# Optimization experiments

Measured on AMD Instinct MI355X. Metric: run time of the kernel, lower is better.

The kernel has to match this reference:

```python
import jax, jax.numpy as jnp
import numpy as np

H = 512  # hidden_size


def setup_inputs() -> dict:
    key = jax.random.key(0)
    ks = jax.random.split(key, 13)
    B, S, E, V = 64, 2048, 512, 32000
    s = 0.05
    return {
        "word_input": jax.random.randint(ks[0], (B,), 0, V),
        "last_hidden": jax.random.normal(ks[1], (1, B, H), jnp.float32),
        "encoder_outputs": jax.random.normal(ks[2], (S, B, H), jnp.float32),
        "emb": jax.random.normal(ks[3], (V, E), jnp.float32) * s,
        "attn_W": jax.random.normal(ks[4], (H, 2 * H), jnp.float32) * s,
        "attn_b": jax.random.normal(ks[5], (H,), jnp.float32) * s,
        "v": jax.random.normal(ks[6], (H,), jnp.float32) * s,
        "W_ih": jax.random.normal(ks[7], (3 * H, H + E), jnp.float32) * s,
        "W_hh": jax.random.normal(ks[8], (3 * H, H), jnp.float32) * s,
        "b_ih": jax.random.normal(ks[9], (3 * H,), jnp.float32) * s,
        "b_hh": jax.random.normal(ks[10], (3 * H,), jnp.float32) * s,
        "out_W": jax.random.normal(ks[11], (V, 2 * H), jnp.float32) * s,
        "out_b": jax.random.normal(ks[12], (V,), jnp.float32) * s,
    }


def reference(word_input, last_hidden, encoder_outputs, emb, attn_W, attn_b, v,
              W_ih, W_hh, b_ih, b_hh, out_W, out_b):
    # word_input: [B] int; last_hidden: [1,B,H]; encoder_outputs: [S,B,H]
    hid = last_hidden[-1]                       # [B,H]
    enc = jnp.transpose(encoder_outputs, (1, 0, 2))  # [B,S,H]

    # Bahdanau 'concat' attention: tanh(W [h;e] + b) . v  (split W to avoid [B,S,2H])
    Wa, We = attn_W[:, :H], attn_W[:, H:]
    energy = jnp.tanh((hid @ Wa.T)[:, None, :] + jnp.einsum('bsh,kh->bsk', enc, We) + attn_b)
    scores = jnp.einsum('bsk,k->bs', energy, v)       # [B,S]
    attn = jax.nn.softmax(scores, axis=1)             # [B,S]
    context = jnp.einsum('bs,bsh->bh', attn, enc)     # [B,H]

    # GRU step (PyTorch gate layout: r, z, n)
    x = jnp.concatenate([emb[word_input], context], axis=1)  # [B,E+H]
    gi = x @ W_ih.T + b_ih
    gh = hid @ W_hh.T + b_hh
    r = jax.nn.sigmoid(gi[:, :H] + gh[:, :H])
    z = jax.nn.sigmoid(gi[:, H:2 * H] + gh[:, H:2 * H])
    n = jnp.tanh(gi[:, 2 * H:] + r * gh[:, 2 * H:])
    h_new = (1.0 - z) * n + z * hid                   # [B,H]

    logits = jnp.concatenate([h_new, context], axis=1) @ out_W.T + out_b
    output = jax.nn.log_softmax(logits, axis=1)       # [B,V]
    return output, h_new[None]                        # hidden: [1,B,H]
```

## Files before the change

kernel.cpp:

```cpp
#include <hip/hip_runtime.h>
#include <hip/hip_bf16.h>
#include <cstdint>
#include <cstddef>

#define HD 512
#define BB 64
#define SS 2048
#define VV 32000
#define MM (SS*BB)
#define NCH 32

typedef __attribute__((ext_vector_type(8))) short bf16x8;
typedef __attribute__((ext_vector_type(4))) float f32x4;

static __device__ __forceinline__ unsigned pack2(float a, float b) {
    unsigned r;
    asm("v_cvt_pk_bf16_f32 %0, %1, %2" : "=v"(r) : "v"(a), "v"(b));
    return r;
}
static __device__ __forceinline__ float rcp_fast(float x) {
    float r; asm("v_rcp_f32 %0, %1" : "=v"(r) : "v"(x)); return r;
}
static __device__ __forceinline__ float tanh_fast(float x) {
    float e = __expf(2.f * x);
    return 1.f - 2.f * rcp_fast(e + 1.f);
}
static __device__ __forceinline__ float sigmoid_fast(float x) {
    return 1.f / (1.f + __expf(-x));
}
static __device__ __forceinline__ void gload16(const void* g, void* l) {
    __builtin_amdgcn_global_load_lds(
        (const __attribute__((address_space(1))) void*)g,
        (__attribute__((address_space(3))) void*)l, 16, 0, 0);
}

__global__ void prep_kernel(const float* __restrict__ hid,
                            const float* __restrict__ attn_W,
                            const float* __restrict__ attn_b,
                            float* __restrict__ qc,
                            uint4* __restrict__ WeB4) {
    int i = blockIdx.x * 256 + threadIdx.x;
    int n = i >> 6, b = i & 63;
    const float* hrow = hid + b * HD;
    const float* wrow = attn_W + (size_t)n * (2 * HD);
    float acc = 0.f;
    for (int k = 0; k < HD; k += 4) {
        float4 h4 = *(const float4*)(hrow + k);
        float4 w4 = *(const float4*)(wrow + k);
        acc += h4.x * w4.x + h4.y * w4.y + h4.z * w4.z + h4.w * w4.w;
    }
    qc[b * HD + n] = acc + attn_b[n];
    int col = (i << 3) & 511;
    int cc0 = col >> 3;
    const float* src = attn_W + (size_t)n * (2 * HD) + HD + col;
    float4 f0 = *(const float4*)(src);
    float4 f1 = *(const float4*)(src + 4);
    uint4 p;
    p.x = pack2(f0.x, f0.y); p.y = pack2(f0.z, f0.w);
    p.z = pack2(f1.x, f1.y); p.w = pack2(f1.z, f1.w);
    int ccs = (cc0 & ~7) | ((cc0 & 7) ^ (n & 7));
    WeB4[n * 64 + ccs] = p;
}

__global__ __launch_bounds__(512, 2) void fattn_kernel(
    const float* __restrict__ enc,
    const uint4* __restrict__ WeB4,
    const float* __restrict__ qc,
    const float* __restrict__ vvec,
    float* __restrict__ oP,
    float* __restrict__ lP)
{
    __shared__ char smem[8192 + 65536 + 2048 + 256];
    uint4* Ald = (uint4*)smem;
    uint4* Bld = (uint4*)(smem + 8192);
    float (*red)[8] = (float(*)[8])(smem + 8192 + 65536);
    float* p_lds = (float*)(smem + 8192 + 65536 + 2048);
    float* opart = (float*)(smem + 8192);

    const int tid = threadIdx.x;
    const int wv = tid >> 6, lane = tid & 63, l15 = lane & 15, l4 = lane >> 4;
    const int b = blockIdx.x & 63;
    const int c = blockIdx.x >> 6;
    const int s0 = c * 64;

    f32x4 acc[4][4] = {};

    const int arow = tid >> 3;
    const int ac8 = tid & 7;
    const float* aptr = enc + ((size_t)(s0 + arow) * 64 + b) * HD + ac8 * 8;
    const int aslot = arow * 8 + (ac8 ^ (arow & 7));

    const int brow = wv * 8 + (lane >> 3);
    const uint4* bg = WeB4 + (size_t)brow * 64 + (lane & 7);

    float4 pa[2][2];
    pa[0][0] = *(const float4*)(aptr);
    pa[0][1] = *(const float4*)(aptr + 4);
#pragma unroll
    for (int i = 0; i < 8; ++i)
        gload16(bg + (size_t)i * 4096, &Bld[i * 512 + tid]);
    pa[1][0] = *(const float4*)(aptr + 64);
    pa[1][1] = *(const float4*)(aptr + 68);
    {
        uint4 u;
        u.x = pack2(pa[0][0].x, pa[0][0].y);
        u.y = pack2(pa[0][0].z, pa[0][0].w);
        u.z = pack2(pa[0][1].x, pa[0][1].y);
        u.w = pack2(pa[0][1].z, pa[0][1].w);
        Ald[aslot] = u;
    }
    asm volatile("s_waitcnt vmcnt(2) lgkmcnt(0)" ::: "memory");
    __builtin_amdgcn_s_barrier();
    __builtin_amdgcn_sched_barrier(0);

#pragma unroll
    for (int t = 0; t < 8; ++t) {
        const int cur = t & 1;
#pragma unroll
        for (int ks = 0; ks < 2; ++ks) {
            const int chunk = ks * 4 + l4;
            bf16x8 af[4], bfr[4];
#pragma unroll
            for (int mi = 0; mi < 4; ++mi) {
                int row = mi * 16 + l15;
                af[mi] = *(const bf16x8*)&Ald[row * 8 + (chunk ^ (row & 7))];
            }
#pragma unroll
            for (int ni = 0; ni < 4; ++ni) {
                int row = wv * 64 + ni * 16 + l15;
                bfr[ni] = *(const bf16x8*)&Bld[row * 8 + (chunk ^ (row & 7))];
            }
#pragma unroll
            for (int mi = 0; mi < 4; ++mi)
#pragma unroll
                for (int ni = 0; ni < 4; ++ni)
                    acc[mi][ni] = __builtin_amdgcn_mfma_f32_16x16x32_bf16(
                        af[mi], bfr[ni], acc[mi][ni], 0, 0, 0);
        }
        asm volatile("s_waitcnt lgkmcnt(0)" ::: "memory");
        __builtin_amdgcn_s_barrier();
        __builtin_amdgcn_sched_barrier(0);

        if (t < 7) {
#pragma unroll
            for (int i = 0; i < 8; ++i)
                gload16(bg + (size_t)i * 4096 + (t + 1) * 8, &Bld[i * 512 + tid]);
            uint4 u;
            u.x = pack2(pa[cur ^ 1][0].x, pa[cur ^ 1][0].y);
            u.y = pack2(pa[cur ^ 1][0].z, pa[cur ^ 1][0].w);
            u.z = pack2(pa[cur ^ 1][1].x, pa[cur ^ 1][1].y);
            u.w = pack2(pa[cur ^ 1][1].z, pa[cur ^ 1][1].w);
            Ald[aslot] = u;
            if (t < 6) {
                pa[cur][0] = *(const float4*)(aptr + (t + 2) * 64);
                pa[cur][1] = *(const float4*)(aptr + (t + 2) * 64 + 4);
                asm volatile("s_waitcnt vmcnt(2) lgkmcnt(0)" ::: "memory");
            } else {
                asm volatile("s_waitcnt vmcnt(0) lgkmcnt(0)" ::: "memory");
            }
            __builtin_amdgcn_s_barrier();
            __builtin_amdgcn_sched_barrier(0);
        }
    }

    float vv[4], qn[4];
#pragma unroll
    for (int ni = 0; ni < 4; ++ni) {
        int n = wv * 64 + ni * 16 + l15;
        vv[ni] = vvec[n];
        qn[ni] = qc[b * HD + n];
    }
#pragma unroll
    for (int mi = 0; mi < 4; ++mi) {
#pragma unroll
        for (int r = 0; r < 4; ++r) {
            const int rowl = mi * 16 + l4 * 4 + r;
            float s = 0.f;
#pragma unroll
            for (int ni = 0; ni < 4; ++ni)
                s += tanh_fast(acc[mi][ni][r] + qn[ni]) * vv[ni];
#pragma unroll
            for (int msk = 8; msk >= 1; msk >>= 1)
                s += __shfl_xor(s, msk);
            if (l15 == 0) red[rowl][wv] = s;
        }
    }
    __syncthreads();
    if (tid < 64) {
        float t = ((red[tid][0] + red[tid][1]) + (red[tid][2] + red[tid][3]))
                + ((red[tid][4] + red[tid][5]) + (red[tid][6] + red[tid][7]));
        float p = __expf(t);
        p_lds[tid] = p;
        float l = p;
#pragma unroll
        for (int msk = 32; msk >= 1; msk >>= 1) l += __shfl_xor(l, msk);
        if (tid == 0) lP[b * NCH + c] = l;
    }
    __syncthreads();

    float o8[8] = {};
    const float* ebase = enc + ((size_t)(s0 + wv * 8) * 64 + b) * HD + lane * 8;
#pragma unroll
    for (int i = 0; i < 8; ++i) {
        float w = p_lds[wv * 8 + i];
        const float* ep = ebase + (size_t)i * 64 * HD;
        float4 e0 = *(const float4*)(ep);
        float4 e1 = *(const float4*)(ep + 4);
        o8[0] += w * e0.x; o8[1] += w * e0.y; o8[2] += w * e0.z; o8[3] += w * e0.w;
        o8[4] += w * e1.x; o8[5] += w * e1.y; o8[6] += w * e1.z; o8[7] += w * e1.w;
    }
    {
        float4* dst = (float4*)&opart[wv * 512 + lane * 8];
        float4 w0 = {o8[0], o8[1], o8[2], o8[3]};
        float4 w1 = {o8[4], o8[5], o8[6], o8[7]};
        dst[0] = w0; dst[1] = w1;
    }
    __syncthreads();
    float o = 0.f;
#pragma unroll
    for (int w = 0; w < 8; ++w) o += opart[w * 512 + tid];
    oP[((size_t)b * NCH + c) * HD + tid] = o;
}

__global__ void combine_kernel(const float* __restrict__ oP,
                               const float* __restrict__ lP,
                               const int* __restrict__ word,
                               const float* __restrict__ emb,
                               float* __restrict__ x,
                               unsigned* __restrict__ y_bf) {
    const int b = blockIdx.x;
    const int tid = threadIdx.x;
    __shared__ float ctx_lds[512];
    float L = 0.f;
#pragma unroll 8
    for (int c = 0; c < NCH; ++c) L += lP[b * NCH + c];
    float o = 0.f;
#pragma unroll 4
    for (int c = 0; c < NCH; ++c)
        o += oP[((size_t)b * NCH + c) * HD + tid];
    float ctx = o / L;
    x[b * 1024 + HD + tid] = ctx;
    ctx_lds[tid] = ctx;
    x[b * 1024 + tid] = emb[(size_t)word[b] * HD + tid];
    __syncthreads();
    if (tid < 256)
        y_bf[b * 512 + 256 + tid] = pack2(ctx_lds[2 * tid], ctx_lds[2 * tid + 1]);
}

__global__ void gates_kernel(const float* __restrict__ x,
                             const float* __restrict__ hid,
                             const float* __restrict__ W_ih,
                             const float* __restrict__ W_hh,
                             const float* __restrict__ b_ih,
                             const float* __restrict__ b_hh,
                             float* __restrict__ gi, float* __restrict__ gh) {
    const int tid = threadIdx.x;
    const int b = tid & 63;
    const int j = blockIdx.x * 4 + (tid >> 6);
    float agi = 0.f, agh = 0.f;
    const float* xr = x + b * 1024;
    const float* wr = W_ih + (size_t)j * 1024;
    for (int k = 0; k < 1024; k += 4) {
        float4 xv = *(const float4*)(xr + k);
        float4 w4 = *(const float4*)(wr + k);
        agi += xv.x * w4.x + xv.y * w4.y + xv.z * w4.z + xv.w * w4.w;
    }
    const float* hr = hid + b * HD;
    const float* wh = W_hh + (size_t)j * HD;
    for (int k = 0; k < HD; k += 4) {
        float4 hv = *(const float4*)(hr + k);
        float4 w4 = *(const float4*)(wh + k);
        agh += hv.x * w4.x + hv.y * w4.y + hv.z * w4.z + hv.w * w4.w;
    }
    gi[b * 1536 + j] = agi + b_ih[j];
    gh[b * 1536 + j] = agh + b_hh[j];
}

__global__ void hnew_kernel(const float* __restrict__ gi,
                            const float* __restrict__ gh,
                            const float* __restrict__ hid,
                            float* __restrict__ out_h,
                            unsigned* __restrict__ y_bf) {
    const int b = blockIdx.x;
    const int h = threadIdx.x * 2;
    float hn[2];
#pragma unroll
    for (int j = 0; j < 2; ++j) {
        int hh = h + j;
        float r = sigmoid_fast(gi[b * 1536 + hh] + gh[b * 1536 + hh]);
        float z = sigmoid_fast(gi[b * 1536 + 512 + hh] + gh[b * 1536 + 512 + hh]);
        float n = tanh_fast(gi[b * 1536 + 1024 + hh] + r * gh[b * 1536 + 1024 + hh]);
        hn[j] = (1.f - z) * n + z * hid[b * HD + hh];
        out_h[b * HD + hh] = hn[j];
    }
    y_bf[b * 512 + (h >> 1)] = pack2(hn[0], hn[1]);
}

__global__ __launch_bounds__(256, 4) void logits_kernel(
    const unsigned short* __restrict__ y_bf,
    const float* __restrict__ out_W,
    const float* __restrict__ out_b,
    float* __restrict__ logits)
{
    __shared__ uint4 Yld[64 * 8];
    __shared__ uint4 Wld[64 * 8];
    const int tid = threadIdx.x;
    const int wv = tid >> 6, lane = tid & 63, l15 = lane & 15, l4 = lane >> 4;
    const int n0 = blockIdx.x * 64;

    f32x4 acc[4] = {};

    const int s1 = tid, s2 = tid + 256;
    const int r1 = s1 >> 3, g1 = (s1 & 7) ^ (r1 & 7);
    const int r2 = s2 >> 3, g2 = (s2 & 7) ^ (r2 & 7);
    const unsigned short* ya1 = y_bf + (size_t)r1 * 1024 + g1 * 8;
    const unsigned short* ya2 = y_bf + (size_t)r2 * 1024 + g2 * 8;

    const int wr = tid >> 3, wc8 = tid & 7;
    const int wsl = wc8 ^ (wr & 7);
    const float* wp0 = out_W + (size_t)(n0 + wr) * 1024 + wc8 * 8;
    const float* wp1 = out_W + (size_t)(n0 + wr + 32) * 1024 + wc8 * 8;

    float4 pw[2][4];
    pw[0][0] = *(const float4*)(wp0);
    pw[0][1] = *(const float4*)(wp0 + 4);
    pw[0][2] = *(const float4*)(wp1);
    pw[0][3] = *(const float4*)(wp1 + 4);

#pragma unroll
    for (int t = 0; t < 16; ++t) {
        const int cur = t & 1;
        if (t > 0) {
            asm volatile("s_waitcnt lgkmcnt(0)" ::: "memory");
            __builtin_amdgcn_s_barrier();
            __builtin_amdgcn_sched_barrier(0);
        }
        gload16(ya1 + t * 64, &Yld[s1]);
        gload16(ya2 + t * 64, &Yld[s2]);
        {
            uint4 u;
            u.x = pack2(pw[cur][0].x, pw[cur][0].y);
            u.y = pack2(pw[cur][0].z, pw[cur][0].w);
            u.z = pack2(pw[cur][1].x, pw[cur][1].y);
            u.w = pack2(pw[cur][1].z, pw[cur][1].w);
            Wld[wr * 8 + wsl] = u;
            u.x = pack2(pw[cur][2].x, pw[cur][2].y);
            u.y = pack2(pw[cur][2].z, pw[cur][2].w);
            u.z = pack2(pw[cur][3].x, pw[cur][3].y);
            u.w = pack2(pw[cur][3].z, pw[cur][3].w);
            Wld[(wr + 32) * 8 + wsl] = u;
        }
        if (t < 15) {
            const int k1 = (t + 1) * 64;
            pw[cur ^ 1][0] = *(const float4*)(wp0 + k1);
            pw[cur ^ 1][1] = *(const float4*)(wp0 + k1 + 4);
            pw[cur ^ 1][2] = *(const float4*)(wp1 + k1);
            pw[cur ^ 1][3] = *(const float4*)(wp1 + k1 + 4);
            asm volatile("s_waitcnt vmcnt(4) lgkmcnt(0)" ::: "memory");
        } else {
            asm volatile("s_waitcnt vmcnt(0) lgkmcnt(0)" ::: "memory");
        }
        __builtin_amdgcn_s_barrier();
        __builtin_amdgcn_sched_barrier(0);

#pragma unroll
        for (int ks = 0; ks < 2; ++ks) {
            const int chunk = ks * 4 + l4;
            bf16x8 af[4], bfr;
#pragma unroll
            for (int mi = 0; mi < 4; ++mi) {
                int row = mi * 16 + l15;
                af[mi] = *(const bf16x8*)&Yld[row * 8 + (chunk ^ (row & 7))];
            }
            {
                int row = wv * 16 + l15;
                bfr = *(const bf16x8*)&Wld[row * 8 + (chunk ^ (row & 7))];
            }
#pragma unroll
            for (int mi = 0; mi < 4; ++mi)
                acc[mi] = __builtin_amdgcn_mfma_f32_16x16x32_bf16(
                    af[mi], bfr, acc[mi], 0, 0, 0);
        }
    }
#pragma unroll
    for (int mi = 0; mi < 4; ++mi) {
#pragma unroll
        for (int r = 0; r < 4; ++r) {
            const int b = mi * 16 + l4 * 4 + r;
            int n = n0 + wv * 16 + l15;
            logits[(size_t)b * VV + n] = acc[mi][r] + out_b[n];
        }
    }
}

__global__ void lsm_kernel(float* __restrict__ logits) {
    const int b = blockIdx.x;
    const int tid = threadIdx.x;
    __shared__ float sm[1024];
    float* row = logits + (size_t)b * VV;
    float m = -1e30f;
    for (int i = tid; i < VV; i += 1024) m = fmaxf(m, row[i]);
    sm[tid] = m; __syncthreads();
    for (int o = 512; o > 0; o >>= 1) {
        if (tid < o) sm[tid] = fmaxf(sm[tid], sm[tid + o]);
        __syncthreads();
    }
    m = sm[0]; __syncthreads();
    float s = 0.f;
    for (int i = tid; i < VV; i += 1024) s += __expf(row[i] - m);
    sm[tid] = s; __syncthreads();
    for (int o = 512; o > 0; o >>= 1) {
        if (tid < o) sm[tid] += sm[tid + o];
        __syncthreads();
    }
    float lse = m + __logf(sm[0]);
    for (int i = tid; i < VV; i += 1024) row[i] -= lse;
}

extern "C" void kernel_launch(void* const* d_in, const int* in_sizes, int n_in,
                              void* d_out, int out_size, void* d_ws, size_t ws_size,
                              hipStream_t stream) {
    (void)in_sizes; (void)n_in; (void)out_size; (void)ws_size;
    const int*   word   = (const int*)d_in[0];
    const float* hid    = (const float*)d_in[1];
    const float* enc    = (const float*)d_in[2];
    const float* emb    = (const float*)d_in[3];
    const float* attn_W = (const float*)d_in[4];
    const float* attn_b = (const float*)d_in[5];
    const float* v      = (const float*)d_in[6];
    const float* W_ih   = (const float*)d_in[7];
    const float* W_hh   = (const float*)d_in[8];
    const float* b_ih   = (const float*)d_in[9];
    const float* b_hh   = (const float*)d_in[10];
    const float* out_W  = (const float*)d_in[11];
    const float* out_b  = (const float*)d_in[12];

    float* out    = (float*)d_out;
    float* logits = out;
    float* out_h  = out + (size_t)BB * VV;

    char* ws0 = (char*)d_ws;
    size_t off = 0;
    float* qc      = (float*)(ws0 + off);    off += 64 * 512 * 4;
    uint4* WeB4    = (uint4*)(ws0 + off);    off += 512 * 512 * 2;
    float* oP      = (float*)(ws0 + off);    off += (size_t)BB * NCH * HD * 4;
    float* lP      = (float*)(ws0 + off);    off += BB * NCH * 4;
    float* x       = (float*)(ws0 + off);    off += 64 * 1024 * 4;
    unsigned* y_bf = (unsigned*)(ws0 + off); off += 64 * 1024 * 2;
    float* gi      = (float*)(ws0 + off);    off += 64 * 1536 * 4;
    float* gh      = (float*)(ws0 + off);    off += 64 * 1536 * 4;

    prep_kernel<<<128, 256, 0, stream>>>(hid, attn_W, attn_b, qc, WeB4);
    fattn_kernel<<<BB * NCH, 512, 0, stream>>>(enc, WeB4, qc, v, oP, lP);
    combine_kernel<<<BB, 512, 0, stream>>>(oP, lP, word, emb, x, y_bf);
    gates_kernel<<<384, 256, 0, stream>>>(x, hid, W_ih, W_hh, b_ih, b_hh, gi, gh);
    hnew_kernel<<<BB, 256, 0, stream>>>(gi, gh, hid, out_h, y_bf);
    logits_kernel<<<VV / 64, 256, 0, stream>>>((const unsigned short*)y_bf, out_W, out_b, logits);
    lsm_kernel<<<BB, 1024, 0, stream>>>(logits);
}
```

Before: 328.2 us.

## Double-buffer attention GEMM LDS with K=32 steps and raise occupancy to 4

Restructures the attention energy GEMM main loop. K is now split into 16 steps of 32 instead of 8 steps of 64. A and B tiles are double-buffered in LDS, with loads prefetched two steps ahead, and a new XOR swizzle covers the narrower 4-chunk rows. The prep kernel stops swizzling WeB4, and the swizzle is applied on the gather side instead. Launch bounds rise to 4 blocks of 512 threads to raise occupancy, which cuts the register budget and risks spills. LDS use is about 74KB per block, which may limit residency anyway.

```diff
diff --git a/kernel.cpp b/kernel.cpp
--- a/kernel.cpp
+++ b/kernel.cpp
@@ -33,6 +33,11 @@
         (const __attribute__((address_space(1))) void*)g,
         (__attribute__((address_space(3))) void*)l, 16, 0, 0);
 }
+
+#define WAITL   asm volatile("s_waitcnt lgkmcnt(0)" ::: "memory")
+#define WAITVL(N) asm volatile("s_waitcnt vmcnt(" #N ") lgkmcnt(0)" ::: "memory")
+#define SBAR    __builtin_amdgcn_s_barrier()
+#define SCHED   __builtin_amdgcn_sched_barrier(0)
 
 __global__ void prep_kernel(const float* __restrict__ hid,
                             const float* __restrict__ attn_W,
@@ -58,11 +63,10 @@
     uint4 p;
     p.x = pack2(f0.x, f0.y); p.y = pack2(f0.z, f0.w);
     p.z = pack2(f1.x, f1.y); p.w = pack2(f1.z, f1.w);
-    int ccs = (cc0 & ~7) | ((cc0 & 7) ^ (n & 7));
-    WeB4[n * 64 + ccs] = p;
-}
-
-__global__ __launch_bounds__(512, 2) void fattn_kernel(
+    WeB4[n * 64 + cc0] = p;
+}
+
+__global__ __launch_bounds__(512, 4) void fattn_kernel(
     const float* __restrict__ enc,
     const uint4* __restrict__ WeB4,
     const float* __restrict__ qc,
@@ -70,11 +74,13 @@
     float* __restrict__ oP,
     float* __restrict__ lP)
 {
-    __shared__ char smem[8192 + 65536 + 2048 + 256];
-    uint4* Ald = (uint4*)smem;
-    uint4* Bld = (uint4*)(smem + 8192);
-    float (*red)[8] = (float(*)[8])(smem + 8192 + 65536);
-    float* p_lds = (float*)(smem + 8192 + 65536 + 2048);
+    __shared__ char smem[76032];
+    uint4* Ald0 = (uint4*)smem;
+    uint4* Ald1 = (uint4*)(smem + 4096);
+    uint4* Bld0 = (uint4*)(smem + 8192);
+    uint4* Bld1 = (uint4*)(smem + 40960);
+    float (*red)[8] = (float(*)[8])(smem + 73728);
+    float* p_lds = (float*)(smem + 75776);
     float* opart = (float*)(smem + 8192);
 
     const int tid = threadIdx.x;
@@ -85,82 +91,65 @@
 
     f32x4 acc[4][4] = {};
 
-    const int arow = tid >> 3;
-    const int ac8 = tid & 7;
-    const float* aptr = enc + ((size_t)(s0 + arow) * 64 + b) * HD + ac8 * 8;
-    const int aslot = arow * 8 + (ac8 ^ (arow & 7));
-
-    const int brow = wv * 8 + (lane >> 3);
-    const uint4* bg = WeB4 + (size_t)brow * 64 + (lane & 7);
-
-    float4 pa[2][2];
-    pa[0][0] = *(const float4*)(aptr);
-    pa[0][1] = *(const float4*)(aptr + 4);
-#pragma unroll
-    for (int i = 0; i < 8; ++i)
-        gload16(bg + (size_t)i * 4096, &Bld[i * 512 + tid]);
-    pa[1][0] = *(const float4*)(aptr + 64);
-    pa[1][1] = *(const float4*)(aptr + 68);
-    {
-        uint4 u;
-        u.x = pack2(pa[0][0].x, pa[0][0].y);
-        u.y = pack2(pa[0][0].z, pa[0][0].w);
-        u.z = pack2(pa[0][1].x, pa[0][1].y);
-        u.w = pack2(pa[0][1].z, pa[0][1].w);
-        Ald[aslot] = u;
-    }
-    asm volatile("s_waitcnt vmcnt(2) lgkmcnt(0)" ::: "memory");
-    __builtin_amdgcn_s_barrier();
-    __builtin_amdgcn_sched_barrier(0);
-
-#pragma unroll
-    for (int t = 0; t < 8; ++t) {
-        const int cur = t & 1;
-#pragma unroll
-        for (int ks = 0; ks < 2; ++ks) {
-            const int chunk = ks * 4 + l4;
-            bf16x8 af[4], bfr[4];
-#pragma unroll
-            for (int mi = 0; mi < 4; ++mi) {
-                int row = mi * 16 + l15;
-                af[mi] = *(const bf16x8*)&Ald[row * 8 + (chunk ^ (row & 7))];
-            }
-#pragma unroll
-            for (int ni = 0; ni < 4; ++ni) {
-                int row = wv * 64 + ni * 16 + l15;
-                bfr[ni] = *(const bf16x8*)&Bld[row * 8 + (chunk ^ (row & 7))];
-            }
-#pragma unroll
-            for (int mi = 0; mi < 4; ++mi)
-#pragma unroll
-                for (int ni = 0; ni < 4; ++ni)
-                    acc[mi][ni] = __builtin_amdgcn_mfma_f32_16x16x32_bf16(
-                        af[mi], bfr[ni], acc[mi][ni], 0, 0, 0);
-        }
-        asm volatile("s_waitcnt lgkmcnt(0)" ::: "memory");
-        __builtin_amdgcn_s_barrier();
-        __builtin_amdgcn_sched_barrier(0);
-
-        if (t < 7) {
-#pragma unroll
-            for (int i = 0; i < 8; ++i)
-                gload16(bg + (size_t)i * 4096 + (t + 1) * 8, &Bld[i * 512 + tid]);
-            uint4 u;
-            u.x = pack2(pa[cur ^ 1][0].x, pa[cur ^ 1][0].y);
-            u.y = pack2(pa[cur ^ 1][0].z, pa[cur ^ 1][0].w);
-            u.z = pack2(pa[cur ^ 1][1].x, pa[cur ^ 1][1].y);
-            u.w = pack2(pa[cur ^ 1][1].z, pa[cur ^ 1][1].w);
-            Ald[aslot] = u;
-            if (t < 6) {
-                pa[cur][0] = *(const float4*)(aptr + (t + 2) * 64);
-                pa[cur][1] = *(const float4*)(aptr + (t + 2) * 64 + 4);
-                asm volatile("s_waitcnt vmcnt(2) lgkmcnt(0)" ::: "memory");
-            } else {
-                asm volatile("s_waitcnt vmcnt(0) lgkmcnt(0)" ::: "memory");
-            }
-            __builtin_amdgcn_s_barrier();
-            __builtin_amdgcn_sched_barrier(0);
-        }
+    const int arow = tid >> 3, ah = tid & 7;
+    const int acl = (ah >> 1) ^ (arow & 3) ^ ((arow >> 2) & 3);
+    const float* aptr = enc + ((size_t)(s0 + arow) * 64 + b) * HD
+                        + acl * 8 + (ah & 1) * 4;
+    const int awslot = arow * 8 + ah;
+
+    int bsrc[4];
+#pragma unroll
+    for (int i = 0; i < 4; ++i) {
+        int L = i * 512 + tid;
+        int br = L >> 2, bcp = L & 3;
+        bsrc[i] = br * 64 + (bcp ^ (br & 3) ^ ((br >> 2) & 3));
+    }
+    const int fsw = l4 ^ (l15 & 3) ^ ((l15 >> 2) & 3);
+
+    float4 paf[2];
+
+#define GLA(T, S)  paf[S] = *(const float4*)(aptr + (T) * 32)
+#define GLB(T, BLD) { _Pragma("unroll") \
+    for (int i = 0; i < 4; ++i) \
+        gload16(WeB4 + bsrc[i] + (T) * 4, &(BLD)[i * 512 + tid]); }
+#define PACKA(S, ALD) { uint2 u2; \
+    u2.x = pack2(paf[S].x, paf[S].y); \
+    u2.y = pack2(paf[S].z, paf[S].w); \
+    ((uint2*)(ALD))[awslot] = u2; }
+#define COMPUTE(ALD, BLD) { bf16x8 af[4], bfr[4]; \
+    _Pragma("unroll") for (int mi = 0; mi < 4; ++mi) \
+        af[mi] = *(const bf16x8*)&(ALD)[(mi * 16 + l15) * 4 + fsw]; \
+    _Pragma("unroll") for (int ni = 0; ni < 4; ++ni) \
+        bfr[ni] = *(const bf16x8*)&(BLD)[(wv * 64 + ni * 16 + l15) * 4 + fsw]; \
+    _Pragma("unroll") for (int mi = 0; mi < 4; ++mi) \
+        _Pragma("unroll") for (int ni = 0; ni < 4; ++ni) \
+            acc[mi][ni] = __builtin_amdgcn_mfma_f32_16x16x32_bf16( \
+                af[mi], bfr[ni], acc[mi][ni], 0, 0, 0); }
+
+    GLA(0, 0);
+    GLB(0, Bld0);
+    GLA(1, 1);
+    GLB(1, Bld1);
+    PACKA(0, Ald0);
+    GLA(2, 0);
+    PACKA(1, Ald1);
+    GLA(3, 1);
+    WAITVL(6);
+    SBAR; SCHED;
+
+#pragma unroll
+    for (int t = 0; t < 16; ++t) {
+        if (t & 1) { COMPUTE(Ald1, Bld1); } else { COMPUTE(Ald0, Bld0); }
+        if (t == 15) break;
+        WAITL; SBAR; SCHED;
+        if (t < 14) { if (t & 1) { GLB(t + 2, Bld1); } else { GLB(t + 2, Bld0); } }
+        if (t < 14) { if (t & 1) { PACKA(1, Ald1); } else { PACKA(0, Ald0); } }
+        if (t < 12) { if (t & 1) { GLA(t + 4, 1); } else { GLA(t + 4, 0); } }
+        if (t <= 11)      { WAITVL(6); }
+        else if (t == 12) { WAITVL(5); }
+        else if (t == 13) { WAITVL(4); }
+        else              { WAITVL(0); }
+        SBAR; SCHED;
     }
 
     float vv[4], qn[4];
@@ -331,9 +320,7 @@
     for (int t = 0; t < 16; ++t) {
         const int cur = t & 1;
         if (t > 0) {
-            asm volatile("s_waitcnt lgkmcnt(0)" ::: "memory");
-            __builtin_amdgcn_s_barrier();
-            __builtin_amdgcn_sched_barrier(0);
+            WAITL; SBAR; SCHED;
         }
         gload16(ya1 + t * 64, &Yld[s1]);
         gload16(ya2 + t * 64, &Yld[s2]);
@@ -356,12 +343,11 @@
             pw[cur ^ 1][1] = *(const float4*)(wp0 + k1 + 4);
             pw[cur ^ 1][2] = *(const float4*)(wp1 + k1);
             pw[cur ^ 1][3] = *(const float4*)(wp1 + k1 + 4);
-            asm volatile("s_waitcnt vmcnt(4) lgkmcnt(0)" ::: "memory");
+            WAITVL(4);
         } else {
-            asm volatile("s_waitcnt vmcnt(0) lgkmcnt(0)" ::: "memory");
-        }
-        __builtin_amdgcn_s_barrier();
-        __builtin_amdgcn_sched_barrier(0);
+            WAITVL(0);
+        }
+        SBAR; SCHED;
 
 #pragma unroll
         for (int ks = 0; ks < 2; ++ks) {
```

Result: slower. 363.4 us (+10.7%).

## Read We fragments directly from global, shrink LDS, split log-softmax across blocks

Applied to the files above, without the earlier changes.

The attention kernel no longer stages the bf16 We weights in LDS. It loads MFMA B fragments straight from global memory (L2-resident, unswizzled) and keeps only the encoder tile in LDS, which shrinks shared memory enough to raise launch bounds to 4 blocks per CU. This trades LDS staging and barrier overhead for higher occupancy, at the risk of global load latency stalling the MFMA loop. The row log-softmax is split into a partial max/sum kernel over 320 blocks and an apply kernel, so more CUs work on the memory-bound pass.

```diff
diff --git a/kernel.cpp b/kernel.cpp
--- a/kernel.cpp
+++ b/kernel.cpp
@@ -33,6 +33,11 @@
         (const __attribute__((address_space(1))) void*)g,
         (__attribute__((address_space(3))) void*)l, 16, 0, 0);
 }
+
+#define WAITL   asm volatile("s_waitcnt lgkmcnt(0)" ::: "memory")
+#define WAITVL(N) asm volatile("s_waitcnt vmcnt(" #N ") lgkmcnt(0)" ::: "memory")
+#define SBAR    __builtin_amdgcn_s_barrier()
+#define SCHED   __builtin_amdgcn_sched_barrier(0)
 
 __global__ void prep_kernel(const float* __restrict__ hid,
                             const float* __restrict__ attn_W,
@@ -58,11 +63,10 @@
     uint4 p;
     p.x = pack2(f0.x, f0.y); p.y = pack2(f0.z, f0.w);
     p.z = pack2(f1.x, f1.y); p.w = pack2(f1.z, f1.w);
-    int ccs = (cc0 & ~7) | ((cc0 & 7) ^ (n & 7));
-    WeB4[n * 64 + ccs] = p;
-}
-
-__global__ __launch_bounds__(512, 2) void fattn_kernel(
+    WeB4[n * 64 + cc0] = p;
+}
+
+__global__ __launch_bounds__(512, 4) void fattn_kernel(
     const float* __restrict__ enc,
     const uint4* __restrict__ WeB4,
     const float* __restrict__ qc,
@@ -70,12 +74,10 @@
     float* __restrict__ oP,
     float* __restrict__ lP)
 {
-    __shared__ char smem[8192 + 65536 + 2048 + 256];
-    uint4* Ald = (uint4*)smem;
-    uint4* Bld = (uint4*)(smem + 8192);
-    float (*red)[8] = (float(*)[8])(smem + 8192 + 65536);
-    float* p_lds = (float*)(smem + 8192 + 65536 + 2048);
-    float* opart = (float*)(smem + 8192);
+    __shared__ uint4 Ald[64 * 8];
+    __shared__ float red[64][8];
+    __shared__ float p_lds[64];
+    __shared__ float opart[8 * 512];
 
     const int tid = threadIdx.x;
     const int wv = tid >> 6, lane = tid & 63, l15 = lane & 15, l4 = lane >> 4;
@@ -90,32 +92,30 @@
     const float* aptr = enc + ((size_t)(s0 + arow) * 64 + b) * HD + ac8 * 8;
     const int aslot = arow * 8 + (ac8 ^ (arow & 7));
 
-    const int brow = wv * 8 + (lane >> 3);
-    const uint4* bg = WeB4 + (size_t)brow * 64 + (lane & 7);
+    const uint4* bbase = WeB4 + (size_t)(wv * 64 + l15) * 64 + l4;
 
     float4 pa[2][2];
     pa[0][0] = *(const float4*)(aptr);
     pa[0][1] = *(const float4*)(aptr + 4);
-#pragma unroll
-    for (int i = 0; i < 8; ++i)
-        gload16(bg + (size_t)i * 4096, &Bld[i * 512 + tid]);
-    pa[1][0] = *(const float4*)(aptr + 64);
-    pa[1][1] = *(const float4*)(aptr + 68);
-    {
-        uint4 u;
-        u.x = pack2(pa[0][0].x, pa[0][0].y);
-        u.y = pack2(pa[0][0].z, pa[0][0].w);
-        u.z = pack2(pa[0][1].x, pa[0][1].y);
-        u.w = pack2(pa[0][1].z, pa[0][1].w);
-        Ald[aslot] = u;
-    }
-    asm volatile("s_waitcnt vmcnt(2) lgkmcnt(0)" ::: "memory");
-    __builtin_amdgcn_s_barrier();
-    __builtin_amdgcn_sched_barrier(0);
 
 #pragma unroll
     for (int t = 0; t < 8; ++t) {
         const int cur = t & 1;
+        if (t > 0) { WAITL; SBAR; SCHED; }
+        {
+            uint4 u;
+            u.x = pack2(pa[cur][0].x, pa[cur][0].y);
+            u.y = pack2(pa[cur][0].z, pa[cur][0].w);
+            u.z = pack2(pa[cur][1].x, pa[cur][1].y);
+            u.w = pack2(pa[cur][1].z, pa[cur][1].w);
+            Ald[aslot] = u;
+        }
+        if (t < 7) {
+            pa[cur ^ 1][0] = *(const float4*)(aptr + (t + 1) * 64);
+            pa[cur ^ 1][1] = *(const float4*)(aptr + (t + 1) * 64 + 4);
+        }
+        WAITL; SBAR; SCHED;
+
 #pragma unroll
         for (int ks = 0; ks < 2; ++ks) {
             const int chunk = ks * 4 + l4;
@@ -126,40 +126,14 @@
                 af[mi] = *(const bf16x8*)&Ald[row * 8 + (chunk ^ (row & 7))];
             }
 #pragma unroll
-            for (int ni = 0; ni < 4; ++ni) {
-                int row = wv * 64 + ni * 16 + l15;
-                bfr[ni] = *(const bf16x8*)&Bld[row * 8 + (chunk ^ (row & 7))];
-            }
+            for (int ni = 0; ni < 4; ++ni)
+                bfr[ni] = *(const bf16x8*)(bbase + ni * 16 * 64 + t * 8 + ks * 4);
 #pragma unroll
             for (int mi = 0; mi < 4; ++mi)
 #pragma unroll
                 for (int ni = 0; ni < 4; ++ni)
                     acc[mi][ni] = __builtin_amdgcn_mfma_f32_16x16x32_bf16(
                         af[mi], bfr[ni], acc[mi][ni], 0, 0, 0);
-        }
-        asm volatile("s_waitcnt lgkmcnt(0)" ::: "memory");
-        __builtin_amdgcn_s_barrier();
-        __builtin_amdgcn_sched_barrier(0);
-
-        if (t < 7) {
-#pragma unroll
-            for (int i = 0; i < 8; ++i)
-                gload16(bg + (size_t)i * 4096 + (t + 1) * 8, &Bld[i * 512 + tid]);
-            uint4 u;
-            u.x = pack2(pa[cur ^ 1][0].x, pa[cur ^ 1][0].y);
-            u.y = pack2(pa[cur ^ 1][0].z, pa[cur ^ 1][0].w);
-            u.z = pack2(pa[cur ^ 1][1].x, pa[cur ^ 1][1].y);
-            u.w = pack2(pa[cur ^ 1][1].z, pa[cur ^ 1][1].w);
-            Ald[aslot] = u;
-            if (t < 6) {
-                pa[cur][0] = *(const float4*)(aptr + (t + 2) * 64);
-                pa[cur][1] = *(const float4*)(aptr + (t + 2) * 64 + 4);
-                asm volatile("s_waitcnt vmcnt(2) lgkmcnt(0)" ::: "memory");
-            } else {
-                asm volatile("s_waitcnt vmcnt(0) lgkmcnt(0)" ::: "memory");
-            }
-            __builtin_amdgcn_s_barrier();
-            __builtin_amdgcn_sched_barrier(0);
         }
     }
 
@@ -331,9 +305,7 @@
     for (int t = 0; t < 16; ++t) {
         const int cur = t & 1;
         if (t > 0) {
-            asm volatile("s_waitcnt lgkmcnt(0)" ::: "memory");
-            __builtin_amdgcn_s_barrier();
-            __builtin_amdgcn_sched_barrier(0);
+            WAITL; SBAR; SCHED;
         }
         gload16(ya1 + t * 64, &Yld[s1]);
         gload16(ya2 + t * 64, &Yld[s2]);
@@ -356,12 +328,11 @@
             pw[cur ^ 1][1] = *(const float4*)(wp0 + k1 + 4);
             pw[cur ^ 1][2] = *(const float4*)(wp1 + k1);
             pw[cur ^ 1][3] = *(const float4*)(wp1 + k1 + 4);
-            asm volatile("s_waitcnt vmcnt(4) lgkmcnt(0)" ::: "memory");
+            WAITVL(4);
         } else {
-            asm volatile("s_waitcnt vmcnt(0) lgkmcnt(0)" ::: "memory");
-        }
-        __builtin_amdgcn_s_barrier();
-        __builtin_amdgcn_sched_barrier(0);
+            WAITVL(0);
+        }
+        SBAR; SCHED;
 
 #pragma unroll
         for (int ks = 0; ks < 2; ++ks) {
@@ -393,28 +364,46 @@
     }
 }
 
-__global__ void lsm_kernel(float* __restrict__ logits) {
-    const int b = blockIdx.x;
-    const int tid = threadIdx.x;
-    __shared__ float sm[1024];
-    float* row = logits + (size_t)b * VV;
+__global__ void lsm1_kernel(const float* __restrict__ logits,
+                            float* __restrict__ part) {
+    const int bid = blockIdx.x;
+    const int b = bid / 5, q = bid - b * 5;
+    const int tid = threadIdx.x;
+    __shared__ float sm[256];
+    const float* row = logits + (size_t)b * VV + q * 6400;
     float m = -1e30f;
-    for (int i = tid; i < VV; i += 1024) m = fmaxf(m, row[i]);
+    for (int i = tid; i < 6400; i += 256) m = fmaxf(m, row[i]);
     sm[tid] = m; __syncthreads();
-    for (int o = 512; o > 0; o >>= 1) {
+    for (int o = 128; o > 0; o >>= 1) {
         if (tid < o) sm[tid] = fmaxf(sm[tid], sm[tid + o]);
         __syncthreads();
     }
     m = sm[0]; __syncthreads();
     float s = 0.f;
-    for (int i = tid; i < VV; i += 1024) s += __expf(row[i] - m);
+    for (int i = tid; i < 6400; i += 256) s += __expf(row[i] - m);
     sm[tid] = s; __syncthreads();
-    for (int o = 512; o > 0; o >>= 1) {
+    for (int o = 128; o > 0; o >>= 1) {
         if (tid < o) sm[tid] += sm[tid + o];
         __syncthreads();
     }
-    float lse = m + __logf(sm[0]);
-    for (int i = tid; i < VV; i += 1024) row[i] -= lse;
+    if (tid == 0) { part[bid * 2] = m; part[bid * 2 + 1] = sm[0]; }
+}
+
+__global__ void lsm2_kernel(float* __restrict__ logits,
+                            const float* __restrict__ part) {
+    const int bid = blockIdx.x;
+    const int b = bid / 5, q = bid - b * 5;
+    const int tid = threadIdx.x;
+    float m = -1e30f;
+#pragma unroll
+    for (int c = 0; c < 5; ++c) m = fmaxf(m, part[(b * 5 + c) * 2]);
+    float L = 0.f;
+#pragma unroll
+    for (int c = 0; c < 5; ++c)
+        L += part[(b * 5 + c) * 2 + 1] * __expf(part[(b * 5 + c) * 2] - m);
+    float lse = m + __logf(L);
+    float* row = logits + (size_t)b * VV + q * 6400;
+    for (int i = tid; i < 6400; i += 256) row[i] -= lse;
 }
 
 extern "C" void kernel_launch(void* const* d_in, const int* in_sizes, int n_in,
@@ -449,6 +438,7 @@
     unsigned* y_bf = (unsigned*)(ws0 + off); off += 64 * 1024 * 2;
     float* gi      = (float*)(ws0 + off);    off += 64 * 1536 * 4;
     float* gh      = (float*)(ws0 + off);    off += 64 * 1536 * 4;
+    float* lsmp    = (float*)(ws0 + off);    off += 320 * 2 * 4;
 
     prep_kernel<<<128, 256, 0, stream>>>(hid, attn_W, attn_b, qc, WeB4);
     fattn_kernel<<<BB * NCH, 512, 0, stream>>>(enc, WeB4, qc, v, oP, lP);
@@ -456,5 +446,6 @@
     gates_kernel<<<384, 256, 0, stream>>>(x, hid, W_ih, W_hh, b_ih, b_hh, gi, gh);
     hnew_kernel<<<BB, 256, 0, stream>>>(gi, gh, hid, out_h, y_bf);
     logits_kernel<<<VV / 64, 256, 0, stream>>>((const unsigned short*)y_bf, out_W, out_b, logits);
-    lsm_kernel<<<BB, 1024, 0, stream>>>(logits);
-}
+    lsm1_kernel<<<320, 256, 0, stream>>>(logits, lsmp);
+    lsm2_kernel<<<320, 256, 0, stream>>>(logits, lsmp);
+}
```

Measured after the change: 373.0 us. 1.14x slower.
